# Kernel tuning notes

Measured on AMD Instinct MI355X. Metric: run time of the kernel, lower is better.

Reference implementation:

```python
import jax, jax.numpy as jnp
import numpy as np

B, T, S, D = 4, 16, 256, 1024
H, HKV = 16, 4
HD = D // H  # 64
N_IMG = 240  # image tokens; remaining S-N_IMG are agent tokens
LOGIT_CAP = 50.0
EPS = 1e-6


def _build_mask():
    # modality-aware mask: image tokens see only image tokens; agent tokens see all
    m = np.zeros((S, S), dtype=bool)
    m[:N_IMG, :N_IMG] = True
    m[N_IMG:, :] = True
    return jnp.asarray(m)


def _build_rope(s, hd):
    half = hd // 2
    inv_freq = 1.0 / (10000.0 ** (np.arange(half, dtype=np.float32) / half))
    pos = np.arange(s, dtype=np.float32)
    ang = np.outer(pos, inv_freq)  # (S, hd/2)
    return jnp.asarray(np.cos(ang)), jnp.asarray(np.sin(ang))


def setup_inputs() -> dict:
    key = jax.random.key(0)
    ks = jax.random.split(key, 7)
    rope_cos, rope_sin = _build_rope(S, HD)
    sc = 0.02
    return {
        "x": jax.random.normal(ks[0], (B, T, S, D), jnp.float32),
        "attn_mask": _build_mask(),
        "rope_cos": rope_cos,
        "rope_sin": rope_sin,
        "Wq": jax.random.normal(ks[1], (D, H * HD), jnp.float32) * sc,
        "Wk": jax.random.normal(ks[2], (D, HKV * HD), jnp.float32) * sc,
        "Wv": jax.random.normal(ks[3], (D, HKV * HD), jnp.float32) * sc,
        "Wo": jax.random.normal(ks[4], (D, D), jnp.float32) * sc,
        "q_scale": jnp.ones((HD,), jnp.float32),
        "k_scale": jnp.ones((HD,), jnp.float32),
    }


def _rmsnorm(t, scale):
    # RMSNorm over head_dim
    var = jnp.mean(jnp.square(t), axis=-1, keepdims=True)
    return t * jax.lax.rsqrt(var + EPS) * scale


def _rope(t, cos, sin):
    # rotate-half RoPE; t: (N, S, h, hd), cos/sin: (S, hd/2)
    half = t.shape[-1] // 2
    t1, t2 = t[..., :half], t[..., half:]
    c = cos[None, :, None, :]
    s = sin[None, :, None, :]
    return jnp.concatenate([t1 * c - t2 * s, t2 * c + t1 * s], axis=-1)


def reference(x, attn_mask, rope_cos, rope_sin, Wq, Wk, Wv, Wo, q_scale, k_scale):
    b, t, s, d = x.shape
    n = b * t
    xf = x.reshape(n, s, d)
    q = (xf @ Wq).reshape(n, s, H, HD)
    k = (xf @ Wk).reshape(n, s, HKV, HD)
    v = (xf @ Wv).reshape(n, s, HKV, HD)
    # QK-norm then RoPE
    q = _rope(_rmsnorm(q, q_scale), rope_cos, rope_sin)
    k = _rope(_rmsnorm(k, k_scale), rope_cos, rope_sin)
    # GQA: repeat kv heads
    rep = H // HKV
    k = jnp.repeat(k, rep, axis=2)
    v = jnp.repeat(v, rep, axis=2)
    scale = 1.0 / jnp.sqrt(jnp.asarray(HD, x.dtype))
    scores = jnp.einsum('nqhd,nkhd->nhqk', q, k) * scale
    # logit soft-capping
    scores = LOGIT_CAP * jnp.tanh(scores / LOGIT_CAP)
    big_neg = jnp.asarray(jnp.finfo(scores.dtype).min, scores.dtype)
    scores = jnp.where(attn_mask[None, None], scores, big_neg)
    p = jax.nn.softmax(scores, axis=-1)
    out = jnp.einsum('nhqk,nkhd->nqhd', p, v).reshape(n, s, d)
    return (out @ Wo).reshape(b, t, s, d)
```

## Files before the change

kernel.cpp:

```cpp
#include <hip/hip_runtime.h>

typedef __bf16 v8bf __attribute__((ext_vector_type(8)));
typedef __bf16 v4bf __attribute__((ext_vector_type(4)));
typedef float floatx4 __attribute__((ext_vector_type(4)));

#define MFMA16(a, b, c) __builtin_amdgcn_mfma_f32_16x16x32_bf16(a, b, c, 0, 0, 0)
#define GLL16(gp, lp)                                                        \
    __builtin_amdgcn_global_load_lds(                                        \
        (const __attribute__((address_space(1))) void*)(gp),                 \
        (__attribute__((address_space(3))) void*)(lp), 16, 0, 0)

__global__ void cast_x(const float* __restrict__ x, __bf16* __restrict__ xb, int n4) {
    int i = blockIdx.x * blockDim.x + threadIdx.x;
    int stride = gridDim.x * blockDim.x;
    for (; i < n4; i += stride) {
        float4 v = ((const float4*)x)[i];
        v4bf o;
        o[0] = (__bf16)v.x; o[1] = (__bf16)v.y; o[2] = (__bf16)v.z; o[3] = (__bf16)v.w;
        ((v4bf*)xb)[i] = o;
    }
}

__global__ void transW(const float* __restrict__ W0, const float* __restrict__ W1,
                       const float* __restrict__ W2, __bf16* __restrict__ dst) {
    __shared__ __bf16 tile[64][65];
    int k0 = blockIdx.x * 64, c0 = blockIdx.y * 64;
    for (int i = threadIdx.x; i < 4096; i += 256) {
        int k = i >> 6, c = i & 63;
        int gc = c0 + c;
        float v;
        if (gc < 1024)      v = W0[(k0 + k) * 1024 + gc];
        else if (gc < 1280) v = W1[(k0 + k) * 256 + gc - 1024];
        else                v = W2[(k0 + k) * 256 + gc - 1280];
        tile[c][k] = (__bf16)v;
    }
    __syncthreads();
    for (int i = threadIdx.x; i < 4096; i += 256) {
        int c = i >> 6, k = i & 63;
        dst[(c0 + c) * 1024 + k0 + k] = tile[c][k];
    }
}

__global__ __launch_bounds__(256) void gemm_bt(const __bf16* __restrict__ A,
                                               const __bf16* __restrict__ B,
                                               __bf16* __restrict__ Cb,
                                               float* __restrict__ Cf,
                                               int N, int K) {
    __shared__ __attribute__((aligned(16))) __bf16 As[128 * 32];
    __shared__ __attribute__((aligned(16))) __bf16 Bs[128 * 32];
    const int t = threadIdx.x, lane = t & 63, w = t >> 6;
    const int m0 = blockIdx.y * 128, n0 = blockIdx.x * 128;
    const int wm = (w >> 1) * 64, wn = (w & 1) * 64;
    const int rl = lane >> 2;
    const int gl = (lane & 3) ^ ((lane >> 3) & 3);
    const __bf16* pA0 = A + (long)(m0 + w * 16 + rl) * K + gl * 8;
    const __bf16* pA1 = A + (long)(m0 + 64 + w * 16 + rl) * K + gl * 8;
    const __bf16* pB0 = B + (long)(n0 + w * 16 + rl) * K + gl * 8;
    const __bf16* pB1 = B + (long)(n0 + 64 + w * 16 + rl) * K + gl * 8;
    __bf16* lA0 = &As[(w * 16) * 32];
    __bf16* lA1 = &As[(64 + w * 16) * 32];
    __bf16* lB0 = &Bs[(w * 16) * 32];
    __bf16* lB1 = &Bs[(64 + w * 16) * 32];
    const int lr = lane & 15, quad = lane >> 4;
    const int ga = ((quad ^ ((lr >> 1) & 3)) * 8);
    floatx4 acc[4][4] = {};
    for (int kk = 0; kk < K; kk += 32) {
        __syncthreads();
        GLL16(pA0 + kk, lA0);
        GLL16(pA1 + kk, lA1);
        GLL16(pB0 + kk, lB0);
        GLL16(pB1 + kk, lB1);
        __syncthreads();
        v8bf af[4], bq[4];
#pragma unroll
        for (int i = 0; i < 4; ++i) af[i] = *(const v8bf*)(&As[(wm + i * 16 + lr) * 32 + ga]);
#pragma unroll
        for (int j = 0; j < 4; ++j) bq[j] = *(const v8bf*)(&Bs[(wn + j * 16 + lr) * 32 + ga]);
#pragma unroll
        for (int i = 0; i < 4; ++i)
#pragma unroll
            for (int j = 0; j < 4; ++j)
                acc[i][j] = MFMA16(af[i], bq[j], acc[i][j]);
    }
#pragma unroll
    for (int i = 0; i < 4; ++i)
#pragma unroll
        for (int j = 0; j < 4; ++j)
#pragma unroll
            for (int r = 0; r < 4; ++r) {
                int row = m0 + wm + i * 16 + (lane >> 4) * 4 + r;
                int col = n0 + wn + j * 16 + (lane & 15);
                if (Cf) Cf[(long)row * N + col] = acc[i][j][r];
                else    Cb[(long)row * N + col] = (__bf16)acc[i][j][r];
            }
}

__global__ __launch_bounds__(256) void qknorm(const __bf16* __restrict__ qkv,
                                              const float* __restrict__ rc,
                                              const float* __restrict__ rs,
                                              const float* __restrict__ qsc,
                                              const float* __restrict__ ksc,
                                              __bf16* __restrict__ Q,
                                              __bf16* __restrict__ Kb) {
    int item = blockIdx.x * 4 + (threadIdx.x >> 6);
    int lane = threadIdx.x & 63;
    int row, col0, s;
    const float* scale;
    __bf16* dst;
    if (item < 262144) {
        row = item >> 4;
        int h = item & 15;
        int n = row >> 8; s = row & 255;
        col0 = h * 64; scale = qsc;
        dst = Q + ((long)((n * 16 + h) * 256) + s) * 64;
    } else {
        int j = item - 262144;
        row = j >> 2;
        int hk = j & 3;
        int n = row >> 8; s = row & 255;
        col0 = 1024 + hk * 64; scale = ksc;
        dst = Kb + ((long)((n * 4 + hk) * 256) + s) * 64;
    }
    float v = (float)qkv[(long)row * 1536 + col0 + lane];
    float sq = v * v;
#pragma unroll
    for (int msk = 1; msk < 64; msk <<= 1) sq += __shfl_xor(sq, msk);
    float rr = rsqrtf(sq * (1.f / 64.f) + 1e-6f);
    v = v * rr * scale[lane];
    float c = rc[s * 32 + (lane & 31)];
    float sn = rs[s * 32 + (lane & 31)];
    float p = __shfl_xor(v, 32);
    v = (lane < 32) ? (v * c - p * sn) : (v * c + p * sn);
    dst[lane] = (__bf16)v;
}

__global__ __launch_bounds__(512) void attn_kernel(const __bf16* __restrict__ Q,
                                                   const __bf16* __restrict__ Kb,
                                                   const __bf16* __restrict__ qkv,
                                                   __bf16* __restrict__ O) {
    __shared__ __attribute__((aligned(16))) __bf16 KV[256 * 64];
    __shared__ __attribute__((aligned(16))) __bf16 Ps[8][16][40];
    const int bx = blockIdx.x;
    const int n = bx >> 5, h = (bx >> 1) & 15, half = bx & 1, hk = h >> 2;
    const int t = threadIdx.x, lane = t & 63, w = t >> 6;
    const int m = lane & 15, quad = lane >> 4;

    for (int p = 0; p < 4; ++p) {
        int l = t + p * 512;
        int s = l >> 3, cg = l & 7;
        v8bf kv = *(const v8bf*)(Kb + ((long)((n * 4 + hk) * 256 + s) << 6) + cg * 8);
        *(v8bf*)(&KV[s * 64 + ((cg ^ (s & 7)) * 8)]) = kv;
    }
    const __bf16* qp = Q + ((long)((n * 16 + h) * 256 + half * 128 + w * 16 + m) << 6) + quad * 8;
    v8bf qa0 = *(const v8bf*)(qp);
    v8bf qa1 = *(const v8bf*)(qp + 32);
    __syncthreads();

    floatx4 sc[16];
#pragma unroll
    for (int ti = 0; ti < 16; ++ti) {
        int srow = ti * 16 + m;
        v8bf b0 = *(const v8bf*)(&KV[srow * 64 + ((quad ^ (srow & 7)) * 8)]);
        v8bf b1 = *(const v8bf*)(&KV[srow * 64 + (((quad + 4) ^ (srow & 7)) * 8)]);
        floatx4 a = {0.f, 0.f, 0.f, 0.f};
        a = MFMA16(qa0, b0, a);
        a = MFMA16(qa1, b1, a);
        sc[ti] = a;
    }

    const int qbase = half * 128 + w * 16 + quad * 4;
    float sum[4] = {0.f, 0.f, 0.f, 0.f};
#pragma unroll
    for (int ti = 0; ti < 16; ++ti)
#pragma unroll
        for (int r = 0; r < 4; ++r) {
            float v = sc[ti][r];
            float e = __builtin_amdgcn_exp2f(v * 0.0072134752f);
            float capped = 50.f - 100.f * __builtin_amdgcn_rcpf(e + 1.f);
            float p = __builtin_amdgcn_exp2f(capped * 1.44269504f);
            if (ti == 15 && (qbase + r) < 240) p = 0.f;
            sc[ti][r] = p;
            sum[r] += p;
        }
    float inv[4];
#pragma unroll
    for (int r = 0; r < 4; ++r) {
#pragma unroll
        for (int msk = 1; msk < 16; msk <<= 1) sum[r] += __shfl_xor(sum[r], msk);
        inv[r] = __builtin_amdgcn_rcpf(sum[r]);
    }

    __syncthreads();
    for (int p = 0; p < 4; ++p) {
        int l = t + p * 512;
        int s = l >> 3, cg = l & 7;
        v8bf vv = *(const v8bf*)(qkv + (long)(n * 256 + s) * 1536 + 1280 + hk * 64 + cg * 8);
#pragma unroll
        for (int j = 0; j < 8; ++j)
            KV[(cg * 8 + j) * 256 + ((s >> 3) ^ j) * 8 + (s & 7)] = vv[j];
    }
    __syncthreads();

    floatx4 oacc[4] = {};
#pragma unroll
    for (int kc = 0; kc < 8; ++kc) {
#pragma unroll
        for (int ht = 0; ht < 2; ++ht) {
            int ti = kc * 2 + ht;
#pragma unroll
            for (int r = 0; r < 4; ++r)
                Ps[w][quad * 4 + r][ht * 16 + m] = (__bf16)sc[ti][r];
        }
        v8bf pa = *(const v8bf*)(&Ps[w][m][quad * 8]);
#pragma unroll
        for (int ct = 0; ct < 4; ++ct) {
            int hd = ct * 16 + m;
            int sg = kc * 4 + quad;
            v8bf vb = *(const v8bf*)(&KV[hd * 256 + ((sg ^ (hd & 7)) * 8)]);
            oacc[ct] = MFMA16(pa, vb, oacc[ct]);
        }
    }
#pragma unroll
    for (int ct = 0; ct < 4; ++ct)
#pragma unroll
        for (int r = 0; r < 4; ++r) {
            int qrow = half * 128 + w * 16 + quad * 4 + r;
            O[(long)(n * 256 + qrow) * 1024 + h * 64 + ct * 16 + m] =
                (__bf16)(oacc[ct][r] * inv[r]);
        }
}

extern "C" void kernel_launch(void* const* d_in, const int* in_sizes, int n_in,
                              void* d_out, int out_size, void* d_ws, size_t ws_size,
                              hipStream_t stream) {
    const float* x  = (const float*)d_in[0];
    const float* rc = (const float*)d_in[2];
    const float* rs = (const float*)d_in[3];
    const float* Wq = (const float*)d_in[4];
    const float* Wk = (const float*)d_in[5];
    const float* Wv = (const float*)d_in[6];
    const float* Wo = (const float*)d_in[7];
    const float* qs = (const float*)d_in[8];
    const float* ks = (const float*)d_in[9];
    float* out = (float*)d_out;
    char* ws = (char*)d_ws;

    __bf16* x_bf    = (__bf16*)(ws);
    __bf16* WqkvT   = (__bf16*)(ws + 33554432);
    __bf16* WoT     = (__bf16*)(ws + 36700160);
    __bf16* qkv_bf  = (__bf16*)(ws + 38797312);
    __bf16* K_bf    = (__bf16*)(ws + 89128960);
    __bf16* attn_bf = (__bf16*)(ws + 97517568);
    __bf16* Q_bf    = x_bf;

    cast_x<<<4096, 256, 0, stream>>>(x, x_bf, 16777216 / 4);
    transW<<<dim3(16, 24), 256, 0, stream>>>(Wq, Wk, Wv, WqkvT);
    transW<<<dim3(16, 16), 256, 0, stream>>>(Wo, Wo, Wo, WoT);
    gemm_bt<<<dim3(12, 128), 256, 0, stream>>>(x_bf, WqkvT, qkv_bf, nullptr, 1536, 1024);
    qknorm<<<81920, 256, 0, stream>>>(qkv_bf, rc, rs, qs, ks, Q_bf, K_bf);
    attn_kernel<<<2048, 512, 0, stream>>>(Q_bf, K_bf, qkv_bf, attn_bf);
    gemm_bt<<<dim3(8, 128), 256, 0, stream>>>(attn_bf, WoT, nullptr, out, 1024, 1024);
}
```

Measured before the change: 377.0 us.

## Fuse Q norm/RoPE into attention, merge weight transposes, deepen GEMM K-step, stage stores

Q RMSNorm and RoPE now run inside the attention kernel straight from the QKV buffer, so the separate norm kernel handles only K and the Q intermediate round trip goes away. The two weight-transpose launches are merged into one. The GEMM now loads 64 K-elements per barrier pair, with K fixed at 1024. Its epilogue stages results through shared memory so global stores are coalesced vector writes. The cost is extra per-lane register work in attention and a larger shared-memory footprint in the GEMM.

```diff
diff --git a/kernel.cpp b/kernel.cpp
--- a/kernel.cpp
+++ b/kernel.cpp
@@ -22,121 +22,136 @@
 }
 
 __global__ void transW(const float* __restrict__ W0, const float* __restrict__ W1,
-                       const float* __restrict__ W2, __bf16* __restrict__ dst) {
+                       const float* __restrict__ W2, const float* __restrict__ W3,
+                       __bf16* __restrict__ dqkv, __bf16* __restrict__ dwo) {
     __shared__ __bf16 tile[64][65];
-    int k0 = blockIdx.x * 64, c0 = blockIdx.y * 64;
+    int k0 = blockIdx.x * 64;
+    int byy = blockIdx.y;
+    bool isO = byy >= 24;
+    int c0 = (isO ? byy - 24 : byy) * 64;
     for (int i = threadIdx.x; i < 4096; i += 256) {
         int k = i >> 6, c = i & 63;
         int gc = c0 + c;
         float v;
-        if (gc < 1024)      v = W0[(k0 + k) * 1024 + gc];
+        if (isO)            v = W3[(k0 + k) * 1024 + gc];
+        else if (gc < 1024) v = W0[(k0 + k) * 1024 + gc];
         else if (gc < 1280) v = W1[(k0 + k) * 256 + gc - 1024];
         else                v = W2[(k0 + k) * 256 + gc - 1280];
         tile[c][k] = (__bf16)v;
     }
     __syncthreads();
+    __bf16* dst = isO ? dwo : dqkv;
     for (int i = threadIdx.x; i < 4096; i += 256) {
         int c = i >> 6, k = i & 63;
         dst[(c0 + c) * 1024 + k0 + k] = tile[c][k];
     }
 }
 
+template <typename OUT>
 __global__ __launch_bounds__(256) void gemm_bt(const __bf16* __restrict__ A,
                                                const __bf16* __restrict__ B,
-                                               __bf16* __restrict__ Cb,
-                                               float* __restrict__ Cf,
-                                               int N, int K) {
-    __shared__ __attribute__((aligned(16))) __bf16 As[128 * 32];
-    __shared__ __attribute__((aligned(16))) __bf16 Bs[128 * 32];
+                                               OUT* __restrict__ C, int N) {
+    __shared__ __attribute__((aligned(16))) __bf16 smem[16384];
+    __bf16* As = smem;
+    __bf16* Bs = smem + 8192;
     const int t = threadIdx.x, lane = t & 63, w = t >> 6;
     const int m0 = blockIdx.y * 128, n0 = blockIdx.x * 128;
     const int wm = (w >> 1) * 64, wn = (w & 1) * 64;
     const int rl = lane >> 2;
     const int gl = (lane & 3) ^ ((lane >> 3) & 3);
-    const __bf16* pA0 = A + (long)(m0 + w * 16 + rl) * K + gl * 8;
-    const __bf16* pA1 = A + (long)(m0 + 64 + w * 16 + rl) * K + gl * 8;
-    const __bf16* pB0 = B + (long)(n0 + w * 16 + rl) * K + gl * 8;
-    const __bf16* pB1 = B + (long)(n0 + 64 + w * 16 + rl) * K + gl * 8;
+    const __bf16* pA0 = A + (long)(m0 + w * 16 + rl) * 1024 + gl * 8;
+    const __bf16* pA1 = A + (long)(m0 + 64 + w * 16 + rl) * 1024 + gl * 8;
+    const __bf16* pB0 = B + (long)(n0 + w * 16 + rl) * 1024 + gl * 8;
+    const __bf16* pB1 = B + (long)(n0 + 64 + w * 16 + rl) * 1024 + gl * 8;
     __bf16* lA0 = &As[(w * 16) * 32];
     __bf16* lA1 = &As[(64 + w * 16) * 32];
     __bf16* lB0 = &Bs[(w * 16) * 32];
     __bf16* lB1 = &Bs[(64 + w * 16) * 32];
-    const int lr = lane & 15, quad = lane >> 4;
+    const int lr = lane & 15, quad = lane >> 4, m = lane & 15;
     const int ga = ((quad ^ ((lr >> 1) & 3)) * 8);
     floatx4 acc[4][4] = {};
-    for (int kk = 0; kk < K; kk += 32) {
+    for (int kk = 0; kk < 1024; kk += 64) {
         __syncthreads();
-        GLL16(pA0 + kk, lA0);
-        GLL16(pA1 + kk, lA1);
-        GLL16(pB0 + kk, lB0);
-        GLL16(pB1 + kk, lB1);
+        GLL16(pA0 + kk, lA0);          GLL16(pA0 + kk + 32, lA0 + 4096);
+        GLL16(pA1 + kk, lA1);          GLL16(pA1 + kk + 32, lA1 + 4096);
+        GLL16(pB0 + kk, lB0);          GLL16(pB0 + kk + 32, lB0 + 4096);
+        GLL16(pB1 + kk, lB1);          GLL16(pB1 + kk + 32, lB1 + 4096);
         __syncthreads();
-        v8bf af[4], bq[4];
-#pragma unroll
-        for (int i = 0; i < 4; ++i) af[i] = *(const v8bf*)(&As[(wm + i * 16 + lr) * 32 + ga]);
-#pragma unroll
-        for (int j = 0; j < 4; ++j) bq[j] = *(const v8bf*)(&Bs[(wn + j * 16 + lr) * 32 + ga]);
-#pragma unroll
-        for (int i = 0; i < 4; ++i)
+#pragma unroll
+        for (int p = 0; p < 2; ++p) {
+            v8bf af[4], bq[4];
+#pragma unroll
+            for (int i = 0; i < 4; ++i)
+                af[i] = *(const v8bf*)(&As[p * 4096 + (wm + i * 16 + lr) * 32 + ga]);
 #pragma unroll
             for (int j = 0; j < 4; ++j)
-                acc[i][j] = MFMA16(af[i], bq[j], acc[i][j]);
-    }
-#pragma unroll
-    for (int i = 0; i < 4; ++i)
-#pragma unroll
-        for (int j = 0; j < 4; ++j)
-#pragma unroll
-            for (int r = 0; r < 4; ++r) {
-                int row = m0 + wm + i * 16 + (lane >> 4) * 4 + r;
-                int col = n0 + wn + j * 16 + (lane & 15);
-                if (Cf) Cf[(long)row * N + col] = acc[i][j][r];
-                else    Cb[(long)row * N + col] = (__bf16)acc[i][j][r];
-            }
-}
-
-__global__ __launch_bounds__(256) void qknorm(const __bf16* __restrict__ qkv,
-                                              const float* __restrict__ rc,
-                                              const float* __restrict__ rs,
-                                              const float* __restrict__ qsc,
-                                              const float* __restrict__ ksc,
-                                              __bf16* __restrict__ Q,
-                                              __bf16* __restrict__ Kb) {
+                bq[j] = *(const v8bf*)(&Bs[p * 4096 + (wn + j * 16 + lr) * 32 + ga]);
+#pragma unroll
+            for (int i = 0; i < 4; ++i)
+#pragma unroll
+                for (int j = 0; j < 4; ++j)
+                    acc[i][j] = MFMA16(af[i], bq[j], acc[i][j]);
+        }
+    }
+    __syncthreads();
+    const int row2 = lane >> 2, cb = lane & 3;
+    if constexpr (sizeof(OUT) == 2) {
+        __bf16* tile = smem + w * (16 * 68);
+#pragma unroll
+        for (int i = 0; i < 4; ++i) {
+#pragma unroll
+            for (int j = 0; j < 4; ++j)
+#pragma unroll
+                for (int r = 0; r < 4; ++r)
+                    tile[(quad * 4 + r) * 68 + j * 16 + m] = (__bf16)acc[i][j][r];
+            __bf16* dst = (__bf16*)C + (long)(m0 + wm + i * 16 + row2) * N + n0 + wn + cb * 16;
+            *(v8bf*)dst = *(const v8bf*)(&tile[row2 * 68 + cb * 16]);
+            *(v8bf*)(dst + 8) = *(const v8bf*)(&tile[row2 * 68 + cb * 16 + 8]);
+        }
+    } else {
+        float* tile = (float*)smem + w * (16 * 66);
+#pragma unroll
+        for (int i = 0; i < 4; ++i) {
+#pragma unroll
+            for (int j = 0; j < 4; ++j)
+#pragma unroll
+                for (int r = 0; r < 4; ++r)
+                    tile[(quad * 4 + r) * 66 + j * 16 + m] = acc[i][j][r];
+            float* dst = (float*)C + (long)(m0 + wm + i * 16 + row2) * N + n0 + wn + cb * 16;
+#pragma unroll
+            for (int c = 0; c < 4; ++c)
+                *(floatx4*)(dst + c * 4) = *(const floatx4*)(&tile[row2 * 66 + cb * 16 + c * 4]);
+        }
+    }
+}
+
+__global__ __launch_bounds__(256) void knorm(const __bf16* __restrict__ qkv,
+                                             const float* __restrict__ rc,
+                                             const float* __restrict__ rs,
+                                             const float* __restrict__ ksc,
+                                             __bf16* __restrict__ Kb) {
     int item = blockIdx.x * 4 + (threadIdx.x >> 6);
     int lane = threadIdx.x & 63;
-    int row, col0, s;
-    const float* scale;
-    __bf16* dst;
-    if (item < 262144) {
-        row = item >> 4;
-        int h = item & 15;
-        int n = row >> 8; s = row & 255;
-        col0 = h * 64; scale = qsc;
-        dst = Q + ((long)((n * 16 + h) * 256) + s) * 64;
-    } else {
-        int j = item - 262144;
-        row = j >> 2;
-        int hk = j & 3;
-        int n = row >> 8; s = row & 255;
-        col0 = 1024 + hk * 64; scale = ksc;
-        dst = Kb + ((long)((n * 4 + hk) * 256) + s) * 64;
-    }
-    float v = (float)qkv[(long)row * 1536 + col0 + lane];
+    int row = item >> 2, hk = item & 3;
+    int n = row >> 8, s = row & 255;
+    float v = (float)qkv[(long)row * 1536 + 1024 + hk * 64 + lane];
     float sq = v * v;
 #pragma unroll
     for (int msk = 1; msk < 64; msk <<= 1) sq += __shfl_xor(sq, msk);
     float rr = rsqrtf(sq * (1.f / 64.f) + 1e-6f);
-    v = v * rr * scale[lane];
+    v = v * rr * ksc[lane];
     float c = rc[s * 32 + (lane & 31)];
     float sn = rs[s * 32 + (lane & 31)];
     float p = __shfl_xor(v, 32);
     v = (lane < 32) ? (v * c - p * sn) : (v * c + p * sn);
-    dst[lane] = (__bf16)v;
-}
-
-__global__ __launch_bounds__(512) void attn_kernel(const __bf16* __restrict__ Q,
+    Kb[((long)((n * 4 + hk) * 256 + s) << 6) + lane] = (__bf16)v;
+}
+
+__global__ __launch_bounds__(512) void attn_kernel(const __bf16* __restrict__ qkv,
                                                    const __bf16* __restrict__ Kb,
-                                                   const __bf16* __restrict__ qkv,
+                                                   const float* __restrict__ rc,
+                                                   const float* __restrict__ rs,
+                                                   const float* __restrict__ qsc,
                                                    __bf16* __restrict__ O) {
     __shared__ __attribute__((aligned(16))) __bf16 KV[256 * 64];
     __shared__ __attribute__((aligned(16))) __bf16 Ps[8][16][40];
@@ -151,17 +166,37 @@
         v8bf kv = *(const v8bf*)(Kb + ((long)((n * 4 + hk) * 256 + s) << 6) + cg * 8);
         *(v8bf*)(&KV[s * 64 + ((cg ^ (s & 7)) * 8)]) = kv;
     }
-    const __bf16* qp = Q + ((long)((n * 16 + h) * 256 + half * 128 + w * 16 + m) << 6) + quad * 8;
-    v8bf qa0 = *(const v8bf*)(qp);
-    v8bf qa1 = *(const v8bf*)(qp + 32);
+    const int srow = half * 128 + w * 16 + m;
+    const __bf16* qp = qkv + (long)(n * 256 + srow) * 1536 + h * 64 + quad * 8;
+    v8bf qr0 = *(const v8bf*)(qp);
+    v8bf qr1 = *(const v8bf*)(qp + 32);
+    float f0[8], f1[8], ss = 0.f;
+#pragma unroll
+    for (int j = 0; j < 8; ++j) {
+        f0[j] = (float)qr0[j]; f1[j] = (float)qr1[j];
+        ss += f0[j] * f0[j] + f1[j] * f1[j];
+    }
+    ss += __shfl_xor(ss, 16);
+    ss += __shfl_xor(ss, 32);
+    float rr = rsqrtf(ss * (1.f / 64.f) + 1e-6f);
+    v8bf qa0, qa1;
+#pragma unroll
+    for (int j = 0; j < 8; ++j) {
+        int hd = quad * 8 + j;
+        float t1 = f0[j] * rr * qsc[hd];
+        float t2 = f1[j] * rr * qsc[32 + hd];
+        float c = rc[srow * 32 + hd], sn = rs[srow * 32 + hd];
+        qa0[j] = (__bf16)(t1 * c - t2 * sn);
+        qa1[j] = (__bf16)(t2 * c + t1 * sn);
+    }
     __syncthreads();
 
     floatx4 sc[16];
 #pragma unroll
     for (int ti = 0; ti < 16; ++ti) {
-        int srow = ti * 16 + m;
-        v8bf b0 = *(const v8bf*)(&KV[srow * 64 + ((quad ^ (srow & 7)) * 8)]);
-        v8bf b1 = *(const v8bf*)(&KV[srow * 64 + (((quad + 4) ^ (srow & 7)) * 8)]);
+        int kr = ti * 16 + m;
+        v8bf b0 = *(const v8bf*)(&KV[kr * 64 + ((quad ^ (kr & 7)) * 8)]);
+        v8bf b1 = *(const v8bf*)(&KV[kr * 64 + (((quad + 4) ^ (kr & 7)) * 8)]);
         floatx4 a = {0.f, 0.f, 0.f, 0.f};
         a = MFMA16(qa0, b0, a);
         a = MFMA16(qa1, b1, a);
@@ -246,18 +281,16 @@
     char* ws = (char*)d_ws;
 
     __bf16* x_bf    = (__bf16*)(ws);
-    __bf16* WqkvT   = (__bf16*)(ws + 33554432);
-    __bf16* WoT     = (__bf16*)(ws + 36700160);
-    __bf16* qkv_bf  = (__bf16*)(ws + 38797312);
-    __bf16* K_bf    = (__bf16*)(ws + 89128960);
-    __bf16* attn_bf = (__bf16*)(ws + 97517568);
-    __bf16* Q_bf    = x_bf;
+    __bf16* WqkvT   = (__bf16*)(ws + (32l << 20));
+    __bf16* WoT     = (__bf16*)(ws + (35l << 20));
+    __bf16* qkv_bf  = (__bf16*)(ws + (37l << 20));
+    __bf16* K_bf    = (__bf16*)(ws + (85l << 20));
+    __bf16* attn_bf = (__bf16*)(ws + (93l << 20));
 
     cast_x<<<4096, 256, 0, stream>>>(x, x_bf, 16777216 / 4);
-    transW<<<dim3(16, 24), 256, 0, stream>>>(Wq, Wk, Wv, WqkvT);
-    transW<<<dim3(16, 16), 256, 0, stream>>>(Wo, Wo, Wo, WoT);
-    gemm_bt<<<dim3(12, 128), 256, 0, stream>>>(x_bf, WqkvT, qkv_bf, nullptr, 1536, 1024);
-    qknorm<<<81920, 256, 0, stream>>>(qkv_bf, rc, rs, qs, ks, Q_bf, K_bf);
-    attn_kernel<<<2048, 512, 0, stream>>>(Q_bf, K_bf, qkv_bf, attn_bf);
-    gemm_bt<<<dim3(8, 128), 256, 0, stream>>>(attn_bf, WoT, nullptr, out, 1024, 1024);
-}
+    transW<<<dim3(16, 40), 256, 0, stream>>>(Wq, Wk, Wv, Wo, WqkvT, WoT);
+    gemm_bt<__bf16><<<dim3(12, 128), 256, 0, stream>>>(x_bf, WqkvT, qkv_bf, 1536);
+    knorm<<<16384, 256, 0, stream>>>(qkv_bf, rc, rs, ks, K_bf);
+    attn_kernel<<<2048, 512, 0, stream>>>(qkv_bf, K_bf, rc, rs, qs, attn_bf);
+    gemm_bt<float><<<dim3(8, 128), 256, 0, stream>>>(attn_bf, WoT, out, 1024);
+}
```

Result: faster. 330.8 us (-12.2%).
